# Kernel optimization log

Measured on AMD Instinct MI355X. Metric: run time of the kernel, lower is better.

## Reference

```python
import jax, jax.numpy as jnp
import numpy as np

B, N, DIM = 4, 2048, 1024
H, DH = 16, 64
INNER = H * DH  # 1024
SCALE = DH ** -0.5


def setup_inputs() -> dict:
    key = jax.random.key(0)
    ks = jax.random.split(key, 6)
    s = 0.02
    return {
        "x": jax.random.normal(ks[0], (B, N, DIM), dtype=jnp.float32),
        "Wq": jax.random.normal(ks[1], (DIM, INNER), dtype=jnp.float32) * s,
        "Wk": jax.random.normal(ks[2], (DIM, INNER), dtype=jnp.float32) * s,
        "Wv": jax.random.normal(ks[3], (DIM, INNER), dtype=jnp.float32) * s,
        "Wo": jax.random.normal(ks[4], (INNER, DIM), dtype=jnp.float32) * s,
        "bo": jax.random.normal(ks[5], (DIM,), dtype=jnp.float32) * s,
    }


def reference(x, Wq, Wk, Wv, Wo, bo):
    # q/k/v projections: [B,N,INNER] -> [B,H,N,DH]
    def split_heads(t):
        return t.reshape(B, N, H, DH).transpose(0, 2, 1, 3)

    q = split_heads(x @ Wq)
    k = split_heads(x @ Wk)
    v = split_heads(x @ Wv)

    # scores [B,H,N,N], scaled dot product, softmax over keys (last dim)
    dots = jnp.einsum('bhid,bhjd->bhij', q, k) * SCALE
    attn = jax.nn.softmax(dots, axis=-1)

    out = jnp.einsum('bhij,bhjd->bhid', attn, v)
    out = out.transpose(0, 2, 1, 3).reshape(B, N, INNER)
    return out @ Wo + bo
```

## Files before the change

kernel.cpp:

```cpp
#include <hip/hip_runtime.h>

#define B_SZ   4
#define N_SEQ  2048
#define DIM    1024
#define H_N    16
#define DH     64
#define INNER  1024
#define M_TOK  8192
#define QSCALE 0.1803368801111244f

typedef __attribute__((ext_vector_type(8))) short bf16x8;
typedef __attribute__((ext_vector_type(4))) float f32x4;
typedef __attribute__((ext_vector_type(4))) unsigned int u32x4;

__device__ __forceinline__ unsigned short f2b(float f) {
  union { float f; unsigned u; } v; v.f = f;
  unsigned r = v.u + 0x7fffu + ((v.u >> 16) & 1u);
  return (unsigned short)(r >> 16);
}

__device__ __forceinline__ void gl_lds16(const unsigned short* g, unsigned short* l) {
  __builtin_amdgcn_global_load_lds((const __attribute__((address_space(1))) void*)g,
                                   (__attribute__((address_space(3))) void*)l, 16, 0, 0);
}

__global__ __launch_bounds__(256) void cast_x(const float* __restrict__ x,
                                              unsigned short* __restrict__ xb) {
  int i = (blockIdx.x * 256 + threadIdx.x) * 4;
  float4 v = *(const float4*)(x + i);
  ushort4 o;
  o.x = f2b(v.x); o.y = f2b(v.y); o.z = f2b(v.z); o.w = f2b(v.w);
  *(ushort4*)(xb + i) = o;
}

__global__ __launch_bounds__(256) void trans_w(const float* __restrict__ Wq,
    const float* __restrict__ Wk, const float* __restrict__ Wv,
    const float* __restrict__ Wo, unsigned short* __restrict__ WT) {
  const int z = blockIdx.z;
  const float* W = (z == 0) ? Wq : (z == 1) ? Wk : (z == 2) ? Wv : Wo;
  unsigned short* T = WT + (size_t)z * DIM * INNER;
  __shared__ float tile[64][65];
  const int n0 = blockIdx.x * 64, k0 = blockIdx.y * 64;
  const int tid = threadIdx.x;
#pragma unroll
  for (int it = 0; it < 16; it++) {
    int lin = it * 256 + tid;
    int r = lin >> 6, c = lin & 63;
    tile[r][c] = W[(size_t)(k0 + r) * 1024 + n0 + c];
  }
  __syncthreads();
#pragma unroll
  for (int it = 0; it < 16; it++) {
    int lin = it * 256 + tid;
    int r = lin >> 6, c = lin & 63;
    T[(size_t)(n0 + r) * 1024 + k0 + c] = f2b(tile[c][r]);
  }
}

__global__ __launch_bounds__(256) void qkv_gemm(const unsigned short* __restrict__ xb,
    const unsigned short* __restrict__ WT, unsigned short* __restrict__ QKV) {
  __shared__ __align__(16) unsigned short As[2 * 128 * 32];
  __shared__ __align__(16) unsigned short Bs[2 * 128 * 32];
  const int tid = threadIdx.x;
  const int lane = tid & 63, wv = tid >> 6;
  const int quad = lane >> 4, l16 = lane & 15;
  const int wm = wv >> 1, wn = wv & 1;
  const int m0 = blockIdx.x * 128, n0 = blockIdx.y * 128;
  const unsigned short* Ag = xb + (size_t)m0 * DIM;
  const unsigned short* Bg = WT + (size_t)blockIdx.z * DIM * INNER + (size_t)n0 * DIM;
  unsigned short* Out = QKV + (size_t)blockIdx.z * M_TOK * INNER;

  f32x4 zero = {0.f, 0.f, 0.f, 0.f};
  f32x4 acc[4][4];
#pragma unroll
  for (int i = 0; i < 4; i++)
#pragma unroll
    for (int j = 0; j < 4; j++) acc[i][j] = zero;

  const int lr = lane >> 2, lc = (lane & 3) * 8;
  const int c0 = wv * 2, c1 = wv * 2 + 1;

  for (int k0 = 0; k0 < DIM; k0 += 64) {
    __syncthreads();
#pragma unroll
    for (int h = 0; h < 2; h++) {
      gl_lds16(&Ag[(size_t)(c0 * 16 + lr) * DIM + k0 + h * 32 + lc], &As[h * 4096 + c0 * 512]);
      gl_lds16(&Ag[(size_t)(c1 * 16 + lr) * DIM + k0 + h * 32 + lc], &As[h * 4096 + c1 * 512]);
      gl_lds16(&Bg[(size_t)(c0 * 16 + lr) * DIM + k0 + h * 32 + lc], &Bs[h * 4096 + c0 * 512]);
      gl_lds16(&Bg[(size_t)(c1 * 16 + lr) * DIM + k0 + h * 32 + lc], &Bs[h * 4096 + c1 * 512]);
    }
    __syncthreads();
#pragma unroll
    for (int h = 0; h < 2; h++) {
      bf16x8 af[4], bfr[4];
#pragma unroll
      for (int i = 0; i < 4; i++)
        af[i] = *(const bf16x8*)&As[h * 4096 + (wm * 64 + i * 16 + l16) * 32 + quad * 8];
#pragma unroll
      for (int j = 0; j < 4; j++)
        bfr[j] = *(const bf16x8*)&Bs[h * 4096 + (wn * 64 + j * 16 + l16) * 32 + quad * 8];
#pragma unroll
      for (int i = 0; i < 4; i++)
#pragma unroll
        for (int j = 0; j < 4; j++)
          acc[i][j] = __builtin_amdgcn_mfma_f32_16x16x32_bf16(af[i], bfr[j], acc[i][j], 0, 0, 0);
    }
  }
  if (blockIdx.z != 2) {
    const float cs = (blockIdx.z == 0) ? QSCALE : 1.0f;
#pragma unroll
    for (int i = 0; i < 4; i++) {
#pragma unroll
      for (int j = 0; j < 4; j++) {
        int n = n0 + wn * 64 + j * 16 + l16;
#pragma unroll
        for (int r = 0; r < 4; r++) {
          int m = m0 + wm * 64 + i * 16 + quad * 4 + r;
          Out[(size_t)m * INNER + n] = f2b(acc[i][j][r] * cs);
        }
      }
    }
  } else {
#pragma unroll
    for (int i = 0; i < 4; i++) {
#pragma unroll
      for (int j = 0; j < 4; j++) {
        int n = n0 + wn * 64 + j * 16 + l16;
        int h = n >> 6, dh = n & 63;
        int mbase = m0 + wm * 64 + i * 16 + quad * 4;
        int b = mbase >> 11, nq = mbase & 2047;
        unsigned lo = (unsigned)f2b(acc[i][j][0]) | ((unsigned)f2b(acc[i][j][1]) << 16);
        unsigned hi = (unsigned)f2b(acc[i][j][2]) | ((unsigned)f2b(acc[i][j][3]) << 16);
        uint2 pw; pw.x = lo; pw.y = hi;
        *(uint2*)&Out[((size_t)(b * H_N + h) * DH + dh) * N_SEQ + nq] = pw;
      }
    }
  }
}

#define KT 64
#define LSTR 72

__global__ __launch_bounds__(512, 4) void attn(const unsigned short* __restrict__ Q,
    const unsigned short* __restrict__ K, const unsigned short* __restrict__ VT,
    unsigned short* __restrict__ O) {
  __shared__ __align__(16) unsigned short Ks[2][KT * LSTR];
  __shared__ __align__(16) unsigned short VTs[2][DH * LSTR];
  const int tid = threadIdx.x;
  const int lane = tid & 63, w = tid >> 6;
  const int quad = lane >> 4, l16 = lane & 15;
  const int bh = blockIdx.y;
  const int b = bh >> 4, h = bh & 15;
  const int q0 = blockIdx.x * 256;
  const unsigned short* Qp = Q + ((size_t)b * N_SEQ) * INNER + h * DH;
  const unsigned short* Kp = K + ((size_t)b * N_SEQ) * INNER + h * DH;
  const unsigned short* VTp = VT + (size_t)bh * DH * N_SEQ;

  bf16x8 aq[2][2];
#pragma unroll
  for (int qi = 0; qi < 2; qi++) {
    const unsigned short* qr = Qp + (size_t)(q0 + w * 32 + qi * 16 + l16) * INNER;
    aq[qi][0] = *(const bf16x8*)&qr[quad * 8];
    aq[qi][1] = *(const bf16x8*)&qr[32 + quad * 8];
  }

  bf16x8 vone;
#pragma unroll
  for (int j = 0; j < 8; j++) vone[j] = (short)0x3F80;

  f32x4 zero = {0.f, 0.f, 0.f, 0.f};
  f32x4 oacc[2][4];
  f32x4 lacc[2];
#pragma unroll
  for (int qi = 0; qi < 2; qi++) {
    lacc[qi] = zero;
#pragma unroll
    for (int t = 0; t < 4; t++) oacc[qi][t] = zero;
  }

  const int srow = tid >> 3, scol = (tid & 7) * 8;

  uint4 kreg, vreg;
  kreg = *(const uint4*)&Kp[(size_t)srow * INNER + scol];
  vreg = *(const uint4*)&VTp[(size_t)srow * N_SEQ + scol];

  const int NT = N_SEQ / KT;
  for (int it = 0; it < NT; it++) {
    unsigned short* ks = Ks[it & 1];
    unsigned short* vs = VTs[it & 1];
    *(uint4*)&ks[srow * LSTR + scol] = kreg;
    *(uint4*)&vs[srow * LSTR + scol] = vreg;
    __syncthreads();
    if (it + 1 < NT) {
      const int kn = (it + 1) * KT;
      kreg = *(const uint4*)&Kp[(size_t)(kn + srow) * INNER + scol];
      vreg = *(const uint4*)&VTp[(size_t)srow * N_SEQ + kn + scol];
    }

#pragma unroll
    for (int half = 0; half < 2; half++) {
      f32x4 s[2][2];
#pragma unroll
      for (int t = 0; t < 2; t++)
#pragma unroll
        for (int qi = 0; qi < 2; qi++) s[t][qi] = zero;

#pragma unroll
      for (int kk = 0; kk < 2; kk++) {
#pragma unroll
        for (int t = 0; t < 2; t++) {
          bf16x8 ka = *(const bf16x8*)&ks[((half * 2 + t) * 16 + l16) * LSTR + kk * 32 + quad * 8];
#pragma unroll
          for (int qi = 0; qi < 2; qi++)
            s[t][qi] = __builtin_amdgcn_mfma_f32_16x16x32_bf16(ka, aq[qi][kk], s[t][qi], 0, 0, 0);
        }
      }

      bf16x8 pa[2];
#pragma unroll
      for (int qi = 0; qi < 2; qi++) {
#pragma unroll
        for (int t = 0; t < 2; t++)
#pragma unroll
          for (int r = 0; r < 4; r++)
            s[t][qi][r] = __builtin_amdgcn_exp2f(s[t][qi][r]);
        unsigned lo0, hi0, lo1, hi1;
        asm volatile(
            "v_cvt_pk_bf16_f32 %0, %4, %5\n\t"
            "v_cvt_pk_bf16_f32 %1, %6, %7\n\t"
            "v_cvt_pk_bf16_f32 %2, %8, %9\n\t"
            "v_cvt_pk_bf16_f32 %3, %10, %11\n\t"
            "s_nop 1\n\t"
            "v_permlane32_swap_b32 %0, %2\n\t"
            "v_permlane32_swap_b32 %1, %3\n\t"
            "s_nop 1\n\t"
            "v_permlane16_swap_b32 %0, %2\n\t"
            "v_permlane16_swap_b32 %1, %3\n\t"
            "s_nop 1"
            : "=&v"(lo0), "=&v"(hi0), "=&v"(lo1), "=&v"(hi1)
            : "v"(s[0][qi][0]), "v"(s[0][qi][1]), "v"(s[0][qi][2]), "v"(s[0][qi][3]),
              "v"(s[1][qi][0]), "v"(s[1][qi][1]), "v"(s[1][qi][2]), "v"(s[1][qi][3]));
        u32x4 pk;
        pk.x = lo0; pk.y = hi0; pk.z = lo1; pk.w = hi1;
        pa[qi] = __builtin_bit_cast(bf16x8, pk);
      }

      lacc[0] = __builtin_amdgcn_mfma_f32_16x16x32_bf16(pa[0], vone, lacc[0], 0, 0, 0);
      lacc[1] = __builtin_amdgcn_mfma_f32_16x16x32_bf16(pa[1], vone, lacc[1], 0, 0, 0);
#pragma unroll
      for (int t2 = 0; t2 < 4; t2++) {
        bf16x8 vf = *(const bf16x8*)&vs[(t2 * 16 + l16) * LSTR + half * 32 + quad * 8];
        oacc[0][t2] = __builtin_amdgcn_mfma_f32_16x16x32_bf16(pa[0], vf, oacc[0][t2], 0, 0, 0);
        oacc[1][t2] = __builtin_amdgcn_mfma_f32_16x16x32_bf16(pa[1], vf, oacc[1][t2], 0, 0, 0);
      }
    }
  }

#pragma unroll
  for (int qi = 0; qi < 2; qi++) {
#pragma unroll
    for (int r = 0; r < 4; r++) {
      float rl = __builtin_amdgcn_rcpf(lacc[qi][r]);
      int qrow = q0 + w * 32 + qi * 16 + quad * 4 + r;
#pragma unroll
      for (int t2 = 0; t2 < 4; t2++) {
        int col = h * DH + t2 * 16 + l16;
        O[((size_t)b * N_SEQ + qrow) * INNER + col] = f2b(oacc[qi][t2][r] * rl);
      }
    }
  }
}

__global__ __launch_bounds__(256) void out_gemm(const unsigned short* __restrict__ Ob,
    const unsigned short* __restrict__ WoT, const float* __restrict__ bo,
    float* __restrict__ out) {
  __shared__ __align__(16) unsigned short As[2 * 128 * 32];
  __shared__ __align__(16) unsigned short Bs[2 * 64 * 32];
  const int tid = threadIdx.x;
  const int lane = tid & 63, wv = tid >> 6;
  const int quad = lane >> 4, l16 = lane & 15;
  const int wm = wv >> 1, wn = wv & 1;
  const int m0 = blockIdx.x * 128, n0 = blockIdx.y * 64;
  const unsigned short* Ag = Ob + (size_t)m0 * INNER;
  const unsigned short* Bg = WoT + (size_t)n0 * INNER;

  f32x4 zero = {0.f, 0.f, 0.f, 0.f};
  f32x4 acc[4][2];
#pragma unroll
  for (int i = 0; i < 4; i++)
#pragma unroll
    for (int j = 0; j < 2; j++) acc[i][j] = zero;

  const int lr = lane >> 2, lc = (lane & 3) * 8;
  const int c0 = wv * 2, c1 = wv * 2 + 1;
  const int cb = wv;

  for (int k0 = 0; k0 < INNER; k0 += 64) {
    __syncthreads();
#pragma unroll
    for (int h = 0; h < 2; h++) {
      gl_lds16(&Ag[(size_t)(c0 * 16 + lr) * INNER + k0 + h * 32 + lc], &As[h * 4096 + c0 * 512]);
      gl_lds16(&Ag[(size_t)(c1 * 16 + lr) * INNER + k0 + h * 32 + lc], &As[h * 4096 + c1 * 512]);
      gl_lds16(&Bg[(size_t)(cb * 16 + lr) * INNER + k0 + h * 32 + lc], &Bs[h * 2048 + cb * 512]);
    }
    __syncthreads();
#pragma unroll
    for (int h = 0; h < 2; h++) {
      bf16x8 af[4], bfr[2];
#pragma unroll
      for (int i = 0; i < 4; i++)
        af[i] = *(const bf16x8*)&As[h * 4096 + (wm * 64 + i * 16 + l16) * 32 + quad * 8];
#pragma unroll
      for (int j = 0; j < 2; j++)
        bfr[j] = *(const bf16x8*)&Bs[h * 2048 + (wn * 32 + j * 16 + l16) * 32 + quad * 8];
#pragma unroll
      for (int i = 0; i < 4; i++)
#pragma unroll
        for (int j = 0; j < 2; j++)
          acc[i][j] = __builtin_amdgcn_mfma_f32_16x16x32_bf16(af[i], bfr[j], acc[i][j], 0, 0, 0);
    }
  }
#pragma unroll
  for (int i = 0; i < 4; i++) {
#pragma unroll
    for (int j = 0; j < 2; j++) {
      int n = n0 + wn * 32 + j * 16 + l16;
      float bias = bo[n];
#pragma unroll
      for (int r = 0; r < 4; r++) {
        int m = m0 + wm * 64 + i * 16 + quad * 4 + r;
        out[(size_t)m * DIM + n] = acc[i][j][r] + bias;
      }
    }
  }
}

extern "C" void kernel_launch(void* const* d_in, const int* in_sizes, int n_in,
                              void* d_out, int out_size, void* d_ws, size_t ws_size,
                              hipStream_t stream) {
  const float* x  = (const float*)d_in[0];
  const float* Wq = (const float*)d_in[1];
  const float* Wk = (const float*)d_in[2];
  const float* Wv = (const float*)d_in[3];
  const float* Wo = (const float*)d_in[4];
  const float* bo = (const float*)d_in[5];

  char* ws = (char*)d_ws;
  unsigned short* xb   = (unsigned short*)ws;
  unsigned short* WT   = (unsigned short*)(ws + (size_t)16777216);
  unsigned short* QKV  = (unsigned short*)(ws + (size_t)25165824);
  unsigned short* Obuf = (unsigned short*)(ws + (size_t)75497472);

  cast_x<<<dim3(8192), 256, 0, stream>>>(x, xb);
  trans_w<<<dim3(16, 16, 4), 256, 0, stream>>>(Wq, Wk, Wv, Wo, WT);
  qkv_gemm<<<dim3(64, 8, 3), 256, 0, stream>>>(xb, WT, QKV);
  attn<<<dim3(8, 64), 512, 0, stream>>>(QKV,
                                        QKV + (size_t)M_TOK * INNER,
                                        QKV + (size_t)2 * M_TOK * INNER,
                                        Obuf);
  out_gemm<<<dim3(64, 16), 256, 0, stream>>>(Obuf, WT + (size_t)3 * DIM * INNER, bo,
                                             (float*)d_out);
}
```

Baseline: 262.9 us.

## Double-buffer LDS tiles in QKV and output projection GEMMs

Both projection GEMMs now keep two LDS buffers per operand. The next K-tile's global-to-LDS loads are issued before the MFMA work on the current tile, and one barrier per iteration replaces two. The aim is to hide global load latency behind matrix compute. The cost is double the shared memory per block, 64KB for qkv_gemm, which can lower occupancy. The compiler may also insert conservative waits on the async LDS loads before the tile reads, which would remove the overlap.

```diff
diff --git a/kernel.cpp b/kernel.cpp
--- a/kernel.cpp
+++ b/kernel.cpp
@@ -59,8 +59,8 @@
 
 __global__ __launch_bounds__(256) void qkv_gemm(const unsigned short* __restrict__ xb,
     const unsigned short* __restrict__ WT, unsigned short* __restrict__ QKV) {
-  __shared__ __align__(16) unsigned short As[2 * 128 * 32];
-  __shared__ __align__(16) unsigned short Bs[2 * 128 * 32];
+  __shared__ __align__(16) unsigned short As[2][2 * 128 * 32];
+  __shared__ __align__(16) unsigned short Bs[2][2 * 128 * 32];
   const int tid = threadIdx.x;
   const int lane = tid & 63, wv = tid >> 6;
   const int quad = lane >> 4, l16 = lane & 15;
@@ -80,25 +80,32 @@
   const int lr = lane >> 2, lc = (lane & 3) * 8;
   const int c0 = wv * 2, c1 = wv * 2 + 1;
 
-  for (int k0 = 0; k0 < DIM; k0 += 64) {
+  auto stage = [&](int k0, int bsel) {
+#pragma unroll
+    for (int h = 0; h < 2; h++) {
+      gl_lds16(&Ag[(size_t)(c0 * 16 + lr) * DIM + k0 + h * 32 + lc], &As[bsel][h * 4096 + c0 * 512]);
+      gl_lds16(&Ag[(size_t)(c1 * 16 + lr) * DIM + k0 + h * 32 + lc], &As[bsel][h * 4096 + c1 * 512]);
+      gl_lds16(&Bg[(size_t)(c0 * 16 + lr) * DIM + k0 + h * 32 + lc], &Bs[bsel][h * 4096 + c0 * 512]);
+      gl_lds16(&Bg[(size_t)(c1 * 16 + lr) * DIM + k0 + h * 32 + lc], &Bs[bsel][h * 4096 + c1 * 512]);
+    }
+  };
+
+  stage(0, 0);
+  const int NKT = DIM / 64;
+  for (int kt = 0; kt < NKT; kt++) {
     __syncthreads();
-#pragma unroll
-    for (int h = 0; h < 2; h++) {
-      gl_lds16(&Ag[(size_t)(c0 * 16 + lr) * DIM + k0 + h * 32 + lc], &As[h * 4096 + c0 * 512]);
-      gl_lds16(&Ag[(size_t)(c1 * 16 + lr) * DIM + k0 + h * 32 + lc], &As[h * 4096 + c1 * 512]);
-      gl_lds16(&Bg[(size_t)(c0 * 16 + lr) * DIM + k0 + h * 32 + lc], &Bs[h * 4096 + c0 * 512]);
-      gl_lds16(&Bg[(size_t)(c1 * 16 + lr) * DIM + k0 + h * 32 + lc], &Bs[h * 4096 + c1 * 512]);
-    }
-    __syncthreads();
+    if (kt + 1 < NKT) stage((kt + 1) * 64, (kt + 1) & 1);
+    const unsigned short* as = As[kt & 1];
+    const unsigned short* bs = Bs[kt & 1];
 #pragma unroll
     for (int h = 0; h < 2; h++) {
       bf16x8 af[4], bfr[4];
 #pragma unroll
       for (int i = 0; i < 4; i++)
-        af[i] = *(const bf16x8*)&As[h * 4096 + (wm * 64 + i * 16 + l16) * 32 + quad * 8];
+        af[i] = *(const bf16x8*)&as[h * 4096 + (wm * 64 + i * 16 + l16) * 32 + quad * 8];
 #pragma unroll
       for (int j = 0; j < 4; j++)
-        bfr[j] = *(const bf16x8*)&Bs[h * 4096 + (wn * 64 + j * 16 + l16) * 32 + quad * 8];
+        bfr[j] = *(const bf16x8*)&bs[h * 4096 + (wn * 64 + j * 16 + l16) * 32 + quad * 8];
 #pragma unroll
       for (int i = 0; i < 4; i++)
 #pragma unroll
@@ -274,8 +281,8 @@
 __global__ __launch_bounds__(256) void out_gemm(const unsigned short* __restrict__ Ob,
     const unsigned short* __restrict__ WoT, const float* __restrict__ bo,
     float* __restrict__ out) {
-  __shared__ __align__(16) unsigned short As[2 * 128 * 32];
-  __shared__ __align__(16) unsigned short Bs[2 * 64 * 32];
+  __shared__ __align__(16) unsigned short As[2][2 * 128 * 32];
+  __shared__ __align__(16) unsigned short Bs[2][2 * 64 * 32];
   const int tid = threadIdx.x;
   const int lane = tid & 63, wv = tid >> 6;
   const int quad = lane >> 4, l16 = lane & 15;
@@ -295,24 +302,31 @@
   const int c0 = wv * 2, c1 = wv * 2 + 1;
   const int cb = wv;
 
-  for (int k0 = 0; k0 < INNER; k0 += 64) {
+  auto stage = [&](int k0, int bsel) {
+#pragma unroll
+    for (int h = 0; h < 2; h++) {
+      gl_lds16(&Ag[(size_t)(c0 * 16 + lr) * INNER + k0 + h * 32 + lc], &As[bsel][h * 4096 + c0 * 512]);
+      gl_lds16(&Ag[(size_t)(c1 * 16 + lr) * INNER + k0 + h * 32 + lc], &As[bsel][h * 4096 + c1 * 512]);
+      gl_lds16(&Bg[(size_t)(cb * 16 + lr) * INNER + k0 + h * 32 + lc], &Bs[bsel][h * 2048 + cb * 512]);
+    }
+  };
+
+  stage(0, 0);
+  const int NKT = INNER / 64;
+  for (int kt = 0; kt < NKT; kt++) {
     __syncthreads();
-#pragma unroll
-    for (int h = 0; h < 2; h++) {
-      gl_lds16(&Ag[(size_t)(c0 * 16 + lr) * INNER + k0 + h * 32 + lc], &As[h * 4096 + c0 * 512]);
-      gl_lds16(&Ag[(size_t)(c1 * 16 + lr) * INNER + k0 + h * 32 + lc], &As[h * 4096 + c1 * 512]);
-      gl_lds16(&Bg[(size_t)(cb * 16 + lr) * INNER + k0 + h * 32 + lc], &Bs[h * 2048 + cb * 512]);
-    }
-    __syncthreads();
+    if (kt + 1 < NKT) stage((kt + 1) * 64, (kt + 1) & 1);
+    const unsigned short* as = As[kt & 1];
+    const unsigned short* bs = Bs[kt & 1];
 #pragma unroll
     for (int h = 0; h < 2; h++) {
       bf16x8 af[4], bfr[2];
 #pragma unroll
       for (int i = 0; i < 4; i++)
-        af[i] = *(const bf16x8*)&As[h * 4096 + (wm * 64 + i * 16 + l16) * 32 + quad * 8];
+        af[i] = *(const bf16x8*)&as[h * 4096 + (wm * 64 + i * 16 + l16) * 32 + quad * 8];
 #pragma unroll
       for (int j = 0; j < 2; j++)
-        bfr[j] = *(const bf16x8*)&Bs[h * 2048 + (wn * 32 + j * 16 + l16) * 32 + quad * 8];
+        bfr[j] = *(const bf16x8*)&bs[h * 2048 + (wn * 32 + j * 16 + l16) * 32 + quad * 8];
 #pragma unroll
       for (int i = 0; i < 4; i++)
 #pragma unroll
```

New measurement: 288.1 us. 1.1x slower.
